# Kernel optimization log

Measured on AMD Instinct MI355X. Metric: run time of the kernel, lower is better.

The kernel has to match this reference:

```python
import jax, jax.numpy as jnp
import numpy as np

IN_F, OUT_F = 4096, 4096
RANK, N_EXP, TOP_K = 8, 64, 16
R_DIM = 16
ALPHA = 32
SCALING = ALPHA / TOP_K  # 2.0
B_SZ, SEQ = 4, 4096
BOTTLENECK = N_EXP * RANK  # 512


def setup_inputs() -> dict:
    key = jax.random.key(0)
    kx, ka, kb, kq, kk = jax.random.split(key, 5)
    x = jax.random.normal(kx, (B_SZ, SEQ, IN_F), dtype=jnp.float32)
    # A: kaiming-uniform-like; B: torch inits to zeros but we use small random
    # values so the output / gradients are non-degenerate for kernel testing.
    A_w = jax.random.normal(ka, (BOTTLENECK, IN_F), dtype=jnp.float32) * (1.0 / np.sqrt(IN_F))
    B_w = jax.random.normal(kb, (OUT_F, BOTTLENECK), dtype=jnp.float32) * 0.02
    Wq_w = jax.random.normal(kq, (R_DIM, IN_F), dtype=jnp.float32) * (1.0 / np.sqrt(IN_F))
    keys = jax.random.normal(kk, (N_EXP, R_DIM), dtype=jnp.float32) * 0.01
    return {"x": x, "A_w": A_w, "B_w": B_w, "Wq_w": Wq_w, "keys": keys}


def reference(x, A_w, B_w, Wq_w, keys):
    # dropout p=0 -> identity
    # shared A projection: [b,s,d] @ [d, E*r] -> [b,s,E,r]
    z = jnp.einsum('bsd,ed->bse', x, A_w).reshape(B_SZ, SEQ, N_EXP, RANK)
    # lowrank router: scores = (x @ Wq.T) @ keys.T -> [b,s,E]
    q = jnp.einsum('bsd,rd->bsr', x, Wq_w)
    scores = jnp.einsum('bsr,er->bse', q, keys)
    top_scores, top_idx = jax.lax.top_k(scores, TOP_K)          # [b,s,k]
    top_w = jax.nn.softmax(top_scores, axis=-1)                  # [b,s,k]
    # dense gate [b,s,E] via scatter of softmaxed top-k weights
    gate = jnp.sum(jax.nn.one_hot(top_idx, N_EXP, dtype=top_w.dtype)
                   * top_w[..., None], axis=-2)                  # [b,s,E]
    z_gated = (z * gate[..., None]).reshape(B_SZ, SEQ, BOTTLENECK)
    out = jnp.einsum('bse,oe->bso', z_gated, B_w) * SCALING      # [b,s,out]
    return out
```

## Files before the change

kernel.cpp:

```cpp
#include <hip/hip_runtime.h>
#include <hip/hip_bf16.h>
#include <stdint.h>

#define T_TOK   16384
#define INF     4096
#define OUTF    4096
#define NEXP    64
#define TOPK    16
#define RDIM    16
#define BOT     512

typedef float  f32x4  __attribute__((ext_vector_type(4)));
typedef short  bf16x8 __attribute__((ext_vector_type(8)));

__device__ __forceinline__ unsigned short f2bf(float f) {
    union { float f; unsigned int u; } c; c.f = f;
    unsigned int r = c.u + 0x7fffu + ((c.u >> 16) & 1u);
    return (unsigned short)(r >> 16);
}

__device__ __forceinline__ void gld_lds16(const void* g, void* l) {
    __builtin_amdgcn_global_load_lds(
        (const __attribute__((address_space(1))) unsigned int*)(uintptr_t)g,
        (__attribute__((address_space(3))) unsigned int*)(unsigned int)(uintptr_t)l,
        16, 0, 0);
}

__global__ void __launch_bounds__(256) cast_w(const float* __restrict__ A,
                                              const float* __restrict__ B,
                                              unsigned short* __restrict__ Ab,
                                              unsigned short* __restrict__ Bb) {
    int i = blockIdx.x * 256 + threadIdx.x;
    const int nA = (BOT * INF) / 4;
    const float* src; unsigned short* dst; int k;
    if (i < nA) { src = A; dst = Ab; k = i; }
    else        { src = B; dst = Bb; k = i - nA; }
    f32x4 v = ((const f32x4*)src)[k];
    ushort4 o;
    o.x = f2bf(v.x); o.y = f2bf(v.y); o.z = f2bf(v.z); o.w = f2bf(v.w);
    ((ushort4*)dst)[k] = o;
}

#define RTM 4

__global__ void __launch_bounds__(256) router_kernel(
    const float* __restrict__ x,
    const float* __restrict__ Wq,
    const float* __restrict__ keys,
    unsigned short* __restrict__ xb,
    float* __restrict__ gate)
{
    const int tid  = threadIdx.x;
    const int lane = tid & 63;
    const int wave = tid >> 6;
    const int g    = blockIdx.x * 4 + wave;
    const size_t t0 = (size_t)g * RTM;

    float acc[RDIM][RTM] = {};

    const float*   xp = x  + t0 * INF + lane * 4;
    const float*   wp = Wq + lane * 4;
    unsigned short* xo = xb + t0 * INF + lane * 4;

    #pragma unroll 2
    for (int j = 0; j < 16; ++j) {
        const int d = j * 256;
        f32x4 xv[RTM];
        #pragma unroll
        for (int t = 0; t < RTM; ++t)
            xv[t] = *(const f32x4*)(xp + (size_t)t * INF + d);
        #pragma unroll
        for (int t = 0; t < RTM; ++t) {
            ushort4 bv;
            bv.x = f2bf(xv[t].x); bv.y = f2bf(xv[t].y);
            bv.z = f2bf(xv[t].z); bv.w = f2bf(xv[t].w);
            *(ushort4*)(xo + (size_t)t * INF + d) = bv;
        }
        #pragma unroll
        for (int rh = 0; rh < 2; ++rh) {
            f32x4 wv[8];
            #pragma unroll
            for (int r = 0; r < 8; ++r)
                wv[r] = *(const f32x4*)(wp + (size_t)(rh * 8 + r) * INF + d);
            #pragma unroll
            for (int r = 0; r < 8; ++r) {
                #pragma unroll
                for (int t = 0; t < RTM; ++t)
                    acc[rh * 8 + r][t] += wv[r].x * xv[t].x + wv[r].y * xv[t].y
                                        + wv[r].z * xv[t].z + wv[r].w * xv[t].w;
            }
        }
    }

    #pragma unroll
    for (int off = 1; off < 64; off <<= 1) {
        #pragma unroll
        for (int r = 0; r < RDIM; ++r)
            #pragma unroll
            for (int t = 0; t < RTM; ++t)
                acc[r][t] += __shfl_xor(acc[r][t], off, 64);
    }

    f32x4 kreg[4];
    #pragma unroll
    for (int i = 0; i < 4; ++i)
        kreg[i] = *(const f32x4*)&keys[lane * RDIM + i * 4];

    #pragma unroll
    for (int t = 0; t < RTM; ++t) {
        float s = 0.0f;
        #pragma unroll
        for (int i = 0; i < 4; ++i) {
            s += acc[i*4+0][t] * kreg[i].x + acc[i*4+1][t] * kreg[i].y
               + acc[i*4+2][t] * kreg[i].z + acc[i*4+3][t] * kreg[i].w;
        }
        int rank = 0;
        for (int j = 0; j < 64; ++j) {
            float sj = __shfl(s, j, 64);
            rank += (sj > s || (sj == s && j < lane)) ? 1 : 0;
        }
        float m = s;
        #pragma unroll
        for (int off = 32; off > 0; off >>= 1)
            m = fmaxf(m, __shfl_xor(m, off, 64));
        float e = (rank < TOPK) ? __expf(s - m) : 0.0f;
        float sum = e;
        #pragma unroll
        for (int off = 32; off > 0; off >>= 1)
            sum += __shfl_xor(sum, off, 64);
        gate[(t0 + t) * NEXP + lane] = e / sum;
    }
}

template <int EPI>
__global__ void __launch_bounds__(256) gemm_bt(
    const unsigned short* __restrict__ A,
    const unsigned short* __restrict__ Bm,
    const float* __restrict__ gate,
    unsigned short* __restrict__ Cb,
    float* __restrict__ Cf,
    const int M, const int N, const int K)
{
    constexpr int BM = 128, BN = 128, BK = 32;
    __shared__ __align__(16) unsigned short As[BM * BK];
    __shared__ __align__(16) unsigned short Bs[BN * BK];

    const int tid  = threadIdx.x;
    const int lane = tid & 63;
    const int wave = tid >> 6;
    const int wr = wave >> 1, wc = wave & 1;
    const int bm = blockIdx.y * BM;
    const int bn = blockIdx.x * BN;

    f32x4 acc[4][4] = {};

    const int srow = tid >> 2;
    const int scol = (tid & 3) * 8;
    const unsigned short* Ap = A  + (size_t)(bm + srow) * K + scol;
    const unsigned short* Bp = Bm + (size_t)(bn + srow) * K + scol;
    unsigned short* AsP = &As[tid * 8];
    unsigned short* BsP = &Bs[tid * 8];

    const int fm = lane & 15;
    const int fk = (lane >> 4) * 8;

    for (int k0 = 0; k0 < K; k0 += BK) {
        __syncthreads();
        gld_lds16(Ap,                  AsP);
        gld_lds16(Ap + (size_t)64 * K, AsP + 64 * BK);
        gld_lds16(Bp,                  BsP);
        gld_lds16(Bp + (size_t)64 * K, BsP + 64 * BK);
        Ap += BK; Bp += BK;
        __syncthreads();

        bf16x8 af[4], bfr[4];
        #pragma unroll
        for (int i = 0; i < 4; ++i)
            af[i] = *(const bf16x8*)&As[(wr * 64 + i * 16 + fm) * BK + fk];
        #pragma unroll
        for (int j = 0; j < 4; ++j)
            bfr[j] = *(const bf16x8*)&Bs[(wc * 64 + j * 16 + fm) * BK + fk];
        #pragma unroll
        for (int i = 0; i < 4; ++i)
            #pragma unroll
            for (int j = 0; j < 4; ++j)
                acc[i][j] = __builtin_amdgcn_mfma_f32_16x16x32_bf16(af[i], bfr[j], acc[i][j], 0, 0, 0);
    }

    const int row0 = (lane >> 4) * 4;
    const int col  = lane & 15;
    #pragma unroll
    for (int i = 0; i < 4; ++i) {
        #pragma unroll
        for (int j = 0; j < 4; ++j) {
            const int nn = bn + wc * 64 + j * 16 + col;
            #pragma unroll
            for (int r = 0; r < 4; ++r) {
                const int mm = bm + wr * 64 + i * 16 + row0 + r;
                if (EPI == 0) {
                    float g = gate[(size_t)mm * NEXP + (nn >> 3)];
                    Cb[(size_t)mm * N + nn] = f2bf(acc[i][j][r] * g);
                } else {
                    Cf[(size_t)mm * N + nn] = acc[i][j][r] * 2.0f;
                }
            }
        }
    }
}

extern "C" void kernel_launch(void* const* d_in, const int* in_sizes, int n_in,
                              void* d_out, int out_size, void* d_ws, size_t ws_size,
                              hipStream_t stream) {
    const float* x    = (const float*)d_in[0];
    const float* A_w  = (const float*)d_in[1];
    const float* B_w  = (const float*)d_in[2];
    const float* Wq   = (const float*)d_in[3];
    const float* keys = (const float*)d_in[4];
    float* out = (float*)d_out;

    char* ws = (char*)d_ws;
    unsigned short* xb = (unsigned short*)(ws);
    unsigned short* Ab = (unsigned short*)(ws + 134217728);
    unsigned short* Bb = (unsigned short*)(ws + 138412032);
    float*        gate = (float*)        (ws + 142606336);
    unsigned short* Zg = (unsigned short*)(ws + 146800640);

    cast_w<<<dim3(4096), dim3(256), 0, stream>>>(A_w, B_w, Ab, Bb);
    router_kernel<<<dim3(T_TOK / (RTM * 4)), dim3(256), 0, stream>>>(x, Wq, keys, xb, gate);
    gemm_bt<0><<<dim3(BOT / 128, T_TOK / 128), dim3(256), 0, stream>>>(
        xb, Ab, gate, Zg, nullptr, T_TOK, BOT, INF);
    gemm_bt<1><<<dim3(OUTF / 128, T_TOK / 128), dim3(256), 0, stream>>>(
        Zg, Bb, nullptr, nullptr, out, T_TOK, OUTF, BOT);
}
```

Before: 809.4 us.

## Split-K the A-projection GEMM with XCD-aware block remap and separate gated reduce

```diff
diff --git a/kernel.cpp b/kernel.cpp
--- a/kernel.cpp
+++ b/kernel.cpp
@@ -132,6 +132,101 @@
     }
 }
 
+__global__ void __launch_bounds__(256) gemm_sk(
+    const unsigned short* __restrict__ A,
+    const unsigned short* __restrict__ Bm,
+    float* __restrict__ Cp,
+    const int M, const int N, const int K)
+{
+    constexpr int BM = 128, BN = 128, BK = 32, KSPLIT = 2;
+    __shared__ __align__(16) unsigned short As[BM * BK];
+    __shared__ __align__(16) unsigned short Bs[BN * BK];
+
+    const int flat = blockIdx.x;
+    const int wg   = (flat & 7) * 128 + (flat >> 3);
+    const int bx   = wg & 3;
+    const int ks   = (wg >> 2) & (KSPLIT - 1);
+    const int by   = wg >> 3;
+
+    const int tid  = threadIdx.x;
+    const int lane = tid & 63;
+    const int wave = tid >> 6;
+    const int wr = wave >> 1, wc = wave & 1;
+    const int bm = by * BM;
+    const int bn = bx * BN;
+    const int kchunk = K / KSPLIT;
+
+    f32x4 acc[4][4] = {};
+
+    const int srow = tid >> 2;
+    const int scol = (tid & 3) * 8;
+    const unsigned short* Ap = A  + (size_t)(bm + srow) * K + ks * kchunk + scol;
+    const unsigned short* Bp = Bm + (size_t)(bn + srow) * K + ks * kchunk + scol;
+    unsigned short* AsP = &As[tid * 8];
+    unsigned short* BsP = &Bs[tid * 8];
+
+    const int fm = lane & 15;
+    const int fk = (lane >> 4) * 8;
+
+    for (int k0 = 0; k0 < kchunk; k0 += BK) {
+        __syncthreads();
+        gld_lds16(Ap,                  AsP);
+        gld_lds16(Ap + (size_t)64 * K, AsP + 64 * BK);
+        gld_lds16(Bp,                  BsP);
+        gld_lds16(Bp + (size_t)64 * K, BsP + 64 * BK);
+        Ap += BK; Bp += BK;
+        __syncthreads();
+
+        bf16x8 af[4], bfr[4];
+        #pragma unroll
+        for (int i = 0; i < 4; ++i)
+            af[i] = *(const bf16x8*)&As[(wr * 64 + i * 16 + fm) * BK + fk];
+        #pragma unroll
+        for (int j = 0; j < 4; ++j)
+            bfr[j] = *(const bf16x8*)&Bs[(wc * 64 + j * 16 + fm) * BK + fk];
+        #pragma unroll
+        for (int i = 0; i < 4; ++i)
+            #pragma unroll
+            for (int j = 0; j < 4; ++j)
+                acc[i][j] = __builtin_amdgcn_mfma_f32_16x16x32_bf16(af[i], bfr[j], acc[i][j], 0, 0, 0);
+    }
+
+    const int row0 = (lane >> 4) * 4;
+    const int col  = lane & 15;
+    float* Cpo = Cp + (size_t)ks * M * N;
+    #pragma unroll
+    for (int i = 0; i < 4; ++i) {
+        #pragma unroll
+        for (int j = 0; j < 4; ++j) {
+            const int nn = bn + wc * 64 + j * 16 + col;
+            #pragma unroll
+            for (int r = 0; r < 4; ++r) {
+                const int mm = bm + wr * 64 + i * 16 + row0 + r;
+                Cpo[(size_t)mm * N + nn] = acc[i][j][r];
+            }
+        }
+    }
+}
+
+__global__ void __launch_bounds__(256) reduce_gate_k(
+    const float* __restrict__ Cp,
+    const float* __restrict__ gate,
+    unsigned short* __restrict__ Zg)
+{
+    const size_t i = (size_t)blockIdx.x * 256 + threadIdx.x;
+    f32x4 v = ((const f32x4*)Cp)[i];
+    f32x4 w = ((const f32x4*)(Cp + (size_t)T_TOK * BOT))[i];
+    const int m = (int)(i >> 7);
+    const int e = ((int)i & 127) >> 1;
+    const float g = gate[(size_t)m * NEXP + e];
+    ushort4 o;
+    o.x = f2bf((v.x + w.x) * g);
+    o.y = f2bf((v.y + w.y) * g);
+    o.z = f2bf((v.z + w.z) * g);
+    o.w = f2bf((v.w + w.w) * g);
+    ((ushort4*)Zg)[i] = o;
+}
+
 template <int EPI>
 __global__ void __launch_bounds__(256) gemm_bt(
     const unsigned short* __restrict__ A,
@@ -225,10 +320,12 @@
     float*        gate = (float*)        (ws + 142606336);
     unsigned short* Zg = (unsigned short*)(ws + 146800640);
 
+    float* Cp = out;
+
     cast_w<<<dim3(4096), dim3(256), 0, stream>>>(A_w, B_w, Ab, Bb);
     router_kernel<<<dim3(T_TOK / (RTM * 4)), dim3(256), 0, stream>>>(x, Wq, keys, xb, gate);
-    gemm_bt<0><<<dim3(BOT / 128, T_TOK / 128), dim3(256), 0, stream>>>(
-        xb, Ab, gate, Zg, nullptr, T_TOK, BOT, INF);
+    gemm_sk<<<dim3(1024), dim3(256), 0, stream>>>(xb, Ab, Cp, T_TOK, BOT, INF);
+    reduce_gate_k<<<dim3(T_TOK * BOT / 4 / 256), dim3(256), 0, stream>>>(Cp, gate, Zg);
     gemm_bt<1><<<dim3(OUTF / 128, T_TOK / 128), dim3(256), 0, stream>>>(
         Zg, Bb, nullptr, nullptr, out, T_TOK, OUTF, BOT);
 }
```

Measured after the change: 722.6 us. -10.7%, faster.
